# Performance work log

Measured on AMD Instinct MI355X. Metric: run time of the kernel, lower is better.

Reference implementation:

```python
import jax, jax.numpy as jnp
import numpy as np

L, D, H, DH, W, G, FF = 2, 768, 12, 64, 256, 64, 3072  # W = one-sided window (attention_window=512)
B, S = 2, 4096
NEG = -1e9


def setup_inputs() -> dict:
    key = jax.random.key(0)
    ks = jax.random.split(key, 16)
    inp = {}
    inp['hidden_states'] = jax.random.normal(ks[0], (B, S, D), jnp.float32)
    # HF Longformer convention: <0 masked, >0 global, 0 local. First G tokens are global.
    inp['attention_mask'] = jnp.zeros((B, S), jnp.float32).at[:, :G].set(1.0)
    inp['padding_len'] = 0
    inp['level_hierarchy'] = 0
    def w(k, shape):
        return (jax.random.normal(k, shape, jnp.float32) * 0.02)
    for i, n in enumerate(['Wq', 'Wk', 'Wv', 'Wqg', 'Wkg', 'Wvg', 'Wo']):
        inp[n] = w(ks[1 + i], (L, D, D))
        inp['b' + n[1:].lower()] = jnp.zeros((L, D), jnp.float32)
    inp['Wi'] = w(ks[8], (L, D, FF)); inp['bi'] = jnp.zeros((L, FF), jnp.float32)
    inp['Wo2'] = w(ks[9], (L, FF, D)); inp['bo2'] = jnp.zeros((L, D), jnp.float32)
    for n in ['ln1', 'ln2']:
        inp[n + '_g'] = jnp.ones((L, D), jnp.float32)
        inp[n + '_b'] = jnp.zeros((L, D), jnp.float32)
    return inp


def _ln(x, g, b):
    mu = jnp.mean(x, -1, keepdims=True)
    var = jnp.mean(jnp.square(x - mu), -1, keepdims=True)
    return (x - mu) * jax.lax.rsqrt(var + 1e-5) * g + b


def _chunk3(x, nc, w):
    # x: [..., S, d] -> [..., nc, 3w, d]: keys of chunks (c-1, c, c+1), zero-padded at the ends
    shp = x.shape
    xr = x.reshape(shp[:-2] + (nc, w, shp[-1]))
    pad = [(0, 0)] * xr.ndim
    pad[-3] = (1, 1)
    xp = jnp.pad(xr, pad)
    return jnp.concatenate([xp[..., :-2, :, :], xp[..., 1:-1, :, :], xp[..., 2:, :, :]], axis=-2)


def _layer(h, mask, Wq, bq, Wk, bk, Wv, bv, Wqg, bqg, Wkg, bkg, Wvg, bvg,
           Wo, bo, ln1_g, ln1_b, Wi, bi, Wo2, bo2, ln2_g, ln2_b):
    Bb, Ss, Dd = h.shape
    nc = Ss // W
    scale = 1.0 / np.sqrt(DH)
    def heads(x):
        return x.reshape(Bb, Ss, H, DH).transpose(0, 2, 1, 3)  # [B,H,S,dh]
    q = heads(h @ Wq + bq) * scale
    k = heads(h @ Wk + bk)
    v = heads(h @ Wv + bv)
    # --- sliding-window (banded) attention, chunked ---
    qc = q.reshape(Bb, H, nc, W, DH)
    k3 = _chunk3(k, nc, W)  # [B,H,nc,3W,dh]
    v3 = _chunk3(v, nc, W)
    local = jnp.einsum('bhcid,bhcjd->bhcij', qc, k3)  # [B,H,nc,W,3W]
    i = jnp.arange(W)[:, None]
    j = jnp.arange(3 * W)[None, :]
    band_ok = jnp.abs(j - W - i) <= W                              # [W,3W]
    keypos = jnp.arange(nc)[:, None, None] * W + (j - W)[None]     # [nc,1,3W]
    in_range = (keypos >= 0) & (keypos < Ss)
    # masked and global keys are removed from the windowed attention (handled via global cols)
    key_local = _chunk3((mask == 0).astype(h.dtype)[..., None], nc, W)[..., 0] > 0.5  # [B,nc,3W]
    valid = band_ok[None, None] & in_range[None] & key_local[:, :, None, :]  # [B,nc,W,3W]
    local = jnp.where(valid[:, None], local, NEG)
    # --- global key columns (every token attends to the G global tokens) ---
    kg, vg = k[:, :, :G], v[:, :, :G]
    sg = jnp.einsum('bhsd,bhgd->bhsg', q, kg).reshape(Bb, H, nc, W, G)
    probs = jax.nn.softmax(jnp.concatenate([sg, local], axis=-1), axis=-1)
    pg, pl = probs[..., :G], probs[..., G:]
    out = (jnp.einsum('bhcig,bhgd->bhcid', pg, vg)
           + jnp.einsum('bhcij,bhcjd->bhcid', pl, v3)).reshape(Bb, H, Ss, DH)
    # --- global token rows: full attention with dedicated global projections ---
    qg = heads(h @ Wqg + bqg)[:, :, :G] * scale
    kgf = heads(h @ Wkg + bkg)
    vgf = heads(h @ Wvg + bvg)
    add = jnp.where(mask < 0, NEG, 0.0)[:, None, None, :]
    pgl = jax.nn.softmax(jnp.einsum('bhgd,bhsd->bhgs', qg, kgf) + add, axis=-1)
    out = out.at[:, :, :G].set(jnp.einsum('bhgs,bhsd->bhgd', pgl, vgf))
    out = jnp.where((mask < 0)[:, None, :, None], 0.0, out)
    attn = out.transpose(0, 2, 1, 3).reshape(Bb, Ss, Dd) @ Wo + bo
    h = _ln(attn + h, ln1_g, ln1_b)
    ff = jax.nn.gelu(h @ Wi + bi, approximate=False) @ Wo2 + bo2
    return _ln(ff + h, ln2_g, ln2_b)


def reference(hidden_states, attention_mask, padding_len, level_hierarchy,
              Wq, bq, Wk, bk, Wv, bv, Wqg, bqg, Wkg, bkg, Wvg, bvg,
              Wo, bo, ln1_g, ln1_b, Wi, bi, Wo2, bo2, ln2_g, ln2_b):
    h = hidden_states
    for l in range(L):
        h = _layer(h, attention_mask,
                   Wq[l], bq[l], Wk[l], bk[l], Wv[l], bv[l],
                   Wqg[l], bqg[l], Wkg[l], bkg[l], Wvg[l], bvg[l],
                   Wo[l], bo[l], ln1_g[l], ln1_b[l],
                   Wi[l], bi[l], Wo2[l], bo2[l], ln2_g[l], ln2_b[l])
    if padding_len > 0:
        h = h[:, :-padding_len]
    return h
```

## Files before the change

### kernel.cpp

```cpp
#include <hip/hip_runtime.h>

#define B_ 2
#define S_ 4096
#define D_ 768
#define H_ 12
#define DH_ 64
#define W_ 256
#define G_ 64
#define FF_ 3072
#define L_ 2
#define M_ (B_*S_)
#define NEGV -1e9f
#define NSPLIT 16

typedef short bf16x8 __attribute__((ext_vector_type(8)));
typedef float f32x4 __attribute__((ext_vector_type(4)));
typedef unsigned short u16;
typedef unsigned short u16x4 __attribute__((ext_vector_type(4)));

__device__ __forceinline__ u16 f2bf(float f) {
  union { float f; unsigned u; } a; a.f = f;
  unsigned r = a.u + 0x7FFFu + ((a.u >> 16) & 1u);
  return (u16)(r >> 16);
}
__device__ __forceinline__ float b2f(u16 u) {
  union { unsigned u; float f; } a; a.u = ((unsigned)u) << 16;
  return a.f;
}

__device__ __forceinline__ f32x4 mfma16(bf16x8 a, bf16x8 b, f32x4 c) {
  return __builtin_amdgcn_mfma_f32_16x16x32_bf16(a, b, c, 0, 0, 0);
}

__device__ __forceinline__ void gload16(const u16* g, u16* l) {
  __builtin_amdgcn_global_load_lds((const __attribute__((address_space(1))) void*)g,
                                   (__attribute__((address_space(3))) void*)l, 16, 0, 0);
}

__device__ __forceinline__ int xcd_swz(int bid, int nwg) {
  if ((nwg & 7) == 0) {
    int cpx = nwg >> 3;
    bid = (bid & 7) * cpx + (bid >> 3);
  }
  return bid;
}

struct Ptr7 { const float* p[7]; };
__global__ __launch_bounds__(256) void wtrans7(Ptr7 in, u16* __restrict__ out) {
  __shared__ float tile[32][33];
  int z = blockIdx.z;
  int slab = z >> 1, l = z & 1;
  const float* src = in.p[slab] + (size_t)l * D_ * D_;
  u16* dst = out + (size_t)z * D_ * D_;
  int k0 = blockIdx.y * 32, n0 = blockIdx.x * 32;
  int tx = threadIdx.x, ty = threadIdx.y;
#pragma unroll
  for (int i = 0; i < 4; i++)
    tile[ty + i*8][tx] = src[(size_t)(k0 + ty + i*8) * D_ + n0 + tx];
  __syncthreads();
#pragma unroll
  for (int i = 0; i < 4; i++)
    dst[(size_t)(n0 + ty + i*8) * D_ + k0 + tx] = f2bf(tile[tx][ty + i*8]);
}

__global__ __launch_bounds__(256) void wtrans(const float* __restrict__ in,
                                              u16* __restrict__ out, int K, int N) {
  __shared__ float tile[32][33];
  size_t base = (size_t)blockIdx.z * K * N;
  int k0 = blockIdx.y * 32, n0 = blockIdx.x * 32;
  int tx = threadIdx.x, ty = threadIdx.y;
#pragma unroll
  for (int i = 0; i < 4; i++)
    tile[ty + i*8][tx] = in[base + (size_t)(k0 + ty + i*8) * N + n0 + tx];
  __syncthreads();
#pragma unroll
  for (int i = 0; i < 4; i++)
    out[base + (size_t)(n0 + ty + i*8) * K + k0 + tx] = f2bf(tile[tx][ty + i*8]);
}

__global__ __launch_bounds__(256) void conv_b(const float* __restrict__ in,
                                              u16* __restrict__ outb, int n4) {
  int i = blockIdx.x * 256 + threadIdx.x;
  if (i >= n4) return;
  float4 v = ((const float4*)in)[i];
  u16x4 o;
  o[0] = f2bf(v.x); o[1] = f2bf(v.y); o[2] = f2bf(v.z); o[3] = f2bf(v.w);
  ((u16x4*)outb)[i] = o;
}

template <int MODE>
__device__ __forceinline__ float epi_post(float v) {
  if (MODE == 2) return v * 0.125f;
  if (MODE == 3) {
    float y = 0.79788456f * (v + 0.044715f * v * v * v);
    float e = __expf(fminf(2.f * y, 20.f));
    return v * e / (e + 1.f);
  }
  return v;
}

struct Bias5 { const float* p[5]; };

template <int MODE, int NW>
__global__ __launch_bounds__(512, 1) void gemm256(const u16* __restrict__ A,
                                                  const u16* __restrict__ Wbase,
                                                  Bias5 bp,
                                                  u16* __restrict__ OutBase,
                                                  int Kdim, int Nstride, int l) {
  __shared__ u16 sA[2][256 * 64];
  __shared__ u16 sB[2][256 * 64];
  int gx = gridDim.x;
  int bid = blockIdx.x + blockIdx.y * gx;
  bid = xcd_swz(bid, gx * gridDim.y);
  int bxx = bid % gx, by = bid / gx;
  int bm = by * 256;
  int widx, bn;
  const u16* Bt; u16* Cb; const float* bias;
  if (NW == 5) {
    widx = bxx / 3;
    bn = (bxx % 3) * 256;
    int slab = widx + (widx >= 3 ? 1 : 0);
    Bt = Wbase + ((size_t)slab * L_ + l) * (size_t)D_ * D_;
    Cb = OutBase + (size_t)slab * M_ * D_;
    bias = bp.p[widx];
  } else {
    widx = 0;
    bn = bxx * 256;
    Bt = Wbase; Cb = OutBase; bias = bp.p[0];
  }
  int tid = threadIdx.x;
  int lane = tid & 63, wid = tid >> 6;
  int wr = wid >> 2, wc = wid & 3;
  int lr = lane & 15, lg = lane >> 4;

  const u16* srcA[4]; const u16* srcB[4];
#pragma unroll
  for (int i = 0; i < 4; i++) {
    int f = tid + i * 512;
    int row = f >> 3, slot = f & 7;
    int c8 = slot ^ (row & 7);
    srcA[i] = A + (size_t)(bm + row) * Kdim + c8 * 8;
    srcB[i] = Bt + (size_t)(bn + row) * Kdim + c8 * 8;
  }

  f32x4 acc[8][4] = {};
  int nt = Kdim >> 6;

#pragma unroll
  for (int i = 0; i < 4; i++) {
    gload16(srcA[i], &sA[0][(tid + i * 512) * 8]);
    gload16(srcB[i], &sB[0][(tid + i * 512) * 8]);
  }

  for (int kt = 0; kt < nt; kt++) {
    int cur = kt & 1;
    if (kt + 1 < nt) {
      int k1 = (kt + 1) << 6;
#pragma unroll
      for (int i = 0; i < 4; i++) {
        gload16(srcA[i] + k1, &sA[cur ^ 1][(tid + i * 512) * 8]);
        gload16(srcB[i] + k1, &sB[cur ^ 1][(tid + i * 512) * 8]);
      }
      asm volatile("s_waitcnt vmcnt(8)" ::: "memory");
    } else {
      asm volatile("s_waitcnt vmcnt(0)" ::: "memory");
    }
    __builtin_amdgcn_s_barrier();
    __builtin_amdgcn_sched_barrier(0);

#pragma unroll
    for (int qm = 0; qm < 2; qm++) {
      bf16x8 af[4][2];
#pragma unroll
      for (int mi = 0; mi < 4; mi++)
#pragma unroll
        for (int ks = 0; ks < 2; ks++) {
          int row = wr * 128 + qm * 64 + mi * 16 + lr;
          int c8 = ks * 4 + lg;
          af[mi][ks] = *(const bf16x8*)&sA[cur][row * 64 + ((c8 ^ (row & 7)) * 8)];
        }
#pragma unroll
      for (int qn = 0; qn < 2; qn++) {
        bf16x8 bfr[2][2];
#pragma unroll
        for (int nj = 0; nj < 2; nj++)
#pragma unroll
          for (int ks = 0; ks < 2; ks++) {
            int row = wc * 64 + qn * 32 + nj * 16 + lr;
            int c8 = ks * 4 + lg;
            bfr[nj][ks] = *(const bf16x8*)&sB[cur][row * 64 + ((c8 ^ (row & 7)) * 8)];
          }
        __builtin_amdgcn_s_setprio(1);
#pragma unroll
        for (int mi = 0; mi < 4; mi++)
#pragma unroll
          for (int nj = 0; nj < 2; nj++)
#pragma unroll
            for (int ks = 0; ks < 2; ks++)
              acc[qm * 4 + mi][qn * 2 + nj] =
                  mfma16(af[mi][ks], bfr[nj][ks], acc[qm * 4 + mi][qn * 2 + nj]);
        __builtin_amdgcn_s_setprio(0);
      }
    }
    __builtin_amdgcn_sched_barrier(0);
    __builtin_amdgcn_s_barrier();
  }

  int r0 = bm + wr * 128, c0 = bn + wc * 64;
  int cr = (lane >> 4) * 4, cc = lane & 15;
  float sc = (NW == 5 && widx == 0) ? 0.125f : 1.0f;
#pragma unroll
  for (int nj = 0; nj < 4; nj++) {
    int col = c0 + nj * 16 + cc;
    float bv = bias[col];
#pragma unroll
    for (int mi = 0; mi < 8; mi++)
#pragma unroll
      for (int r = 0; r < 4; r++) {
        size_t off = (size_t)(r0 + mi * 16 + cr + r) * Nstride + col;
        Cb[off] = f2bf(epi_post<MODE>((acc[mi][nj][r] + bv) * sc));
      }
  }
}

template <int MODE>
__global__ __launch_bounds__(256) void gemm_pipe(const u16* __restrict__ A,
                                                 const u16* __restrict__ Bt,
                                                 const float* __restrict__ bias,
                                                 u16* __restrict__ Cb,
                                                 int Ndim, int Kdim, int rowTileStride) {
  __shared__ u16 sA[2][4096];
  __shared__ u16 sB[2][4096];
  int gx = gridDim.x;
  int bid = blockIdx.x + blockIdx.y * gx;
  bid = xcd_swz(bid, gx * gridDim.y);
  int bm = (bid / gx) * rowTileStride * 128;
  int bn = (bid % gx) * 128;
  int tid = threadIdx.x;
  int lane = tid & 63, w = tid >> 6;
  int r0w = (w >> 1) * 64, c0w = (w & 1) * 64;
  int lr = lane & 15, lg = lane >> 4;

  int f0 = tid, l0 = f0 >> 3, s0 = (f0 & 7) ^ (l0 & 7);
  int row0 = (l0 << 1) | (s0 >> 2), c0s = (s0 & 3) * 8;
  int f1 = tid + 256, l1 = f1 >> 3, s1 = (f1 & 7) ^ (l1 & 7);
  int row1 = (l1 << 1) | (s1 >> 2), c1s = (s1 & 3) * 8;
  const u16* A0 = A + (size_t)(bm + row0) * Kdim + c0s;
  const u16* A1 = A + (size_t)(bm + row1) * Kdim + c1s;
  const u16* B0 = Bt + (size_t)(bn + row0) * Kdim + c0s;
  const u16* B1 = Bt + (size_t)(bn + row1) * Kdim + c1s;

  int offa[4], offb[4];
#pragma unroll
  for (int i = 0; i < 4; i++) {
    int ra = r0w + i * 16 + lr;
    int la = ra >> 1, sa = ((ra & 1) << 2) | lg;
    offa[i] = la * 64 + (sa ^ (la & 7)) * 8;
    int rb = c0w + i * 16 + lr;
    int lb = rb >> 1, sb = ((rb & 1) << 2) | lg;
    offb[i] = lb * 64 + (sb ^ (lb & 7)) * 8;
  }

  int nt = Kdim >> 5;
  f32x4 acc[4][4] = {};

  gload16(A0, &sA[0][tid * 8]);
  gload16(A1, &sA[0][tid * 8 + 2048]);
  gload16(B0, &sB[0][tid * 8]);
  gload16(B1, &sB[0][tid * 8 + 2048]);

  for (int t = 0; t < nt; t++) {
    int cur = t & 1;
    if (t + 1 < nt) {
      int k1 = (t + 1) << 5;
      gload16(A0 + k1, &sA[cur ^ 1][tid * 8]);
      gload16(A1 + k1, &sA[cur ^ 1][tid * 8 + 2048]);
      gload16(B0 + k1, &sB[cur ^ 1][tid * 8]);
      gload16(B1 + k1, &sB[cur ^ 1][tid * 8 + 2048]);
      asm volatile("s_waitcnt vmcnt(4)" ::: "memory");
    } else {
      asm volatile("s_waitcnt vmcnt(0)" ::: "memory");
    }
    __builtin_amdgcn_s_barrier();
    __builtin_amdgcn_sched_barrier(0);
    bf16x8 a[4], b[4];
#pragma unroll
    for (int i = 0; i < 4; i++) a[i] = *(const bf16x8*)&sA[cur][offa[i]];
#pragma unroll
    for (int j = 0; j < 4; j++) b[j] = *(const bf16x8*)&sB[cur][offb[j]];
#pragma unroll
    for (int i = 0; i < 4; i++)
#pragma unroll
      for (int j = 0; j < 4; j++)
        acc[i][j] = mfma16(a[i], b[j], acc[i][j]);
    __builtin_amdgcn_sched_barrier(0);
    __builtin_amdgcn_s_barrier();
    __builtin_amdgcn_sched_barrier(0);
  }

  int r0 = bm + r0w, c0 = bn + c0w;
  int cr = (lane >> 4) * 4, cc = lane & 15;
#pragma unroll
  for (int j = 0; j < 4; j++) {
    int col = c0 + j * 16 + cc;
    float bv = bias[col];
#pragma unroll
    for (int i = 0; i < 4; i++)
#pragma unroll
      for (int r = 0; r < 4; r++) {
        size_t off = (size_t)(r0 + i * 16 + cr + r) * Ndim + col;
        Cb[off] = f2bf(epi_post<MODE>(acc[i][j][r] + bv));
      }
  }
}

__global__ __launch_bounds__(128) void attn_local(const u16* __restrict__ qb,
                                                  const u16* __restrict__ kb_,
                                                  const u16* __restrict__ vb,
                                                  const float* __restrict__ mask,
                                                  u16* __restrict__ ao) {
  int bid = blockIdx.x + blockIdx.y * gridDim.x;
  bid = xcd_swz(bid, 1536);
  int cx = bid & 63, bh = bid >> 6;
  int c = cx >> 2, sub = cx & 3;
  int b = bh / H_, h = bh % H_;
  int tid = threadIdx.x;
  int w = tid >> 6, lane = tid & 63;
  int lr = lane & 15, lg = lane >> 4;

  __shared__ u16 vtT[64][72];
  __shared__ u16 plds[2][32][72];
  __shared__ unsigned char vflag[576];

  int base_off = sub * 64;
  int kwin0 = c * W_ - W_;
  for (int i = tid; i < 576; i += 128) {
    int kp = kwin0 + base_off + i;
    vflag[i] = (kp >= 0 && kp < S_ && mask[b * S_ + kp] == 0.0f) ? 1 : 0;
  }

  size_t hoff = (size_t)b * S_ * D_ + h * DH_;
  int qrow0 = c * W_ + base_off + w * 32;
  bf16x8 aq[2][2];
#pragma unroll
  for (int fi = 0; fi < 2; fi++)
#pragma unroll
    for (int ks = 0; ks < 2; ks++)
      aq[fi][ks] = *(const bf16x8*)(qb + hoff + (size_t)(qrow0 + fi * 16 + lr) * D_ + ks * 32 + lg * 8);

  float ls[2][4];
  f32x4 o[2][4] = {};
#pragma unroll
  for (int fi = 0; fi < 2; fi++)
#pragma unroll
    for (int r = 0; r < 4; r++) ls[fi][r] = 0.f;

  int stg_k4 = tid >> 3, stg_j = tid & 7;
  int stg_dh0 = stg_j * 8;

  for (int kb = 0; kb <= 9; kb++) {
    int kstart = 0;
    if (kb > 0) {
      kstart = kwin0 + base_off + (kb - 1) * 64;
      if (kstart + 64 <= 0 || kstart >= S_) continue;
    }
    __syncthreads();
    {
#pragma unroll
      for (int p = 0; p < 4; p++) {
        int key = p * 16 + stg_k4;
        int kp = (kb ? kstart : 0) + key;
        bf16x8 row = *(const bf16x8*)(vb + hoff + (size_t)kp * D_ + stg_dh0);
        u16* basep = &vtT[stg_dh0][key ^ (stg_j << 3)];
#pragma unroll
        for (int e = 0; e < 8; e++) basep[e * 72] = (u16)row[e];
      }
    }
    __syncthreads();

    bf16x8 bk0[4], bk1[4];
#pragma unroll
    for (int nj = 0; nj < 4; nj++) {
      int kp = (kb ? kstart : 0) + nj * 16 + lr;
      const u16* ks8 = kb_ + hoff + (size_t)kp * D_ + lg * 8;
      bk0[nj] = *(const bf16x8*)(ks8);
      bk1[nj] = *(const bf16x8*)(ks8 + 32);
    }
    f32x4 sc[2][4];
#pragma unroll
    for (int fi = 0; fi < 2; fi++)
#pragma unroll
      for (int nj = 0; nj < 4; nj++) {
        f32x4 t = {};
        t = mfma16(aq[fi][0], bk0[nj], t);
        t = mfma16(aq[fi][1], bk1[nj], t);
        sc[fi][nj] = t;
      }

    if (kb >= 2 && kb <= 8) {
#pragma unroll
      for (int nj = 0; nj < 4; nj++) {
        bool kv = vflag[(kb - 1) * 64 + nj * 16 + lr] != 0;
#pragma unroll
        for (int fi = 0; fi < 2; fi++)
#pragma unroll
          for (int r = 0; r < 4; r++)
            sc[fi][nj][r] = kv ? sc[fi][nj][r] : NEGV;
      }
    } else if (kb > 0) {
#pragma unroll
      for (int nj = 0; nj < 4; nj++) {
        int fidx = (kb - 1) * 64 + nj * 16 + lr;
        int koff = base_off + fidx;
        bool kv = vflag[fidx] != 0;
#pragma unroll
        for (int fi = 0; fi < 2; fi++)
#pragma unroll
          for (int r = 0; r < 4; r++) {
            int wq = base_off + w * 32 + fi * 16 + lg * 4 + r;
            if (!(kv && koff >= wq && koff <= wq + 2 * W_)) sc[fi][nj][r] = NEGV;
          }
      }
    }

#pragma unroll
    for (int fi = 0; fi < 2; fi++)
#pragma unroll
      for (int r = 0; r < 4; r++) {
        float ps = 0.f;
#pragma unroll
        for (int nj = 0; nj < 4; nj++) {
          float p = __expf(sc[fi][nj][r]);
          sc[fi][nj][r] = p;
          ps += p;
        }
#pragma unroll
        for (int d = 1; d < 16; d <<= 1) ps += __shfl_xor(ps, d);
        ls[fi][r] += ps;
      }

#pragma unroll
    for (int fi = 0; fi < 2; fi++)
#pragma unroll
      for (int nj = 0; nj < 4; nj++)
#pragma unroll
        for (int r = 0; r < 4; r++)
          plds[w][fi * 16 + lg * 4 + r][nj * 16 + lr] = f2bf(sc[fi][nj][r]);
    asm volatile("s_waitcnt lgkmcnt(0)" ::: "memory");
    __builtin_amdgcn_sched_barrier(0);

    bf16x8 ap[2][2];
#pragma unroll
    for (int fi = 0; fi < 2; fi++)
#pragma unroll
      for (int ks = 0; ks < 2; ks++)
        ap[fi][ks] = *(const bf16x8*)&plds[w][fi * 16 + lr][ks * 32 + lg * 8];
#pragma unroll
    for (int dj = 0; dj < 4; dj++) {
      int xr = ((dj * 16 + lr) >> 3) & 7;
#pragma unroll
      for (int ks = 0; ks < 2; ks++) {
        bf16x8 bv = *(const bf16x8*)&vtT[dj * 16 + lr][(ks * 32 + lg * 8) ^ (xr << 3)];
        o[0][dj] = mfma16(ap[0][ks], bv, o[0][dj]);
        o[1][dj] = mfma16(ap[1][ks], bv, o[1][dj]);
      }
    }
  }

#pragma unroll
  for (int fi = 0; fi < 2; fi++)
#pragma unroll
    for (int dj = 0; dj < 4; dj++)
#pragma unroll
      for (int r = 0; r < 4; r++) {
        int row = qrow0 + fi * 16 + lg * 4 + r;
        float v = o[fi][dj][r] / ls[fi][r];
        ao[hoff + (size_t)row * D_ + dj * 16 + lr] = f2bf(v);
      }
}

__global__ __launch_bounds__(128) void attn_gsplit(const u16* __restrict__ qg,
                                                   const u16* __restrict__ kg,
                                                   const u16* __restrict__ vg,
                                                   float* __restrict__ opart,
                                                   float* __restrict__ lpart) {
  int sp = blockIdx.x, bh = blockIdx.y;
  int b = bh / H_, h = bh % H_;
  int tid = threadIdx.x, w = tid >> 6, lane = tid & 63;
  int lr = lane & 15, lg = lane >> 4;
  __shared__ u16 vtT[64][72];
  __shared__ u16 plds[2][32][72];
  size_t hoff = (size_t)b * S_ * D_ + h * DH_;
  int qrow0 = w * 32;
  bf16x8 aq[2][2];
#pragma unroll
  for (int fi = 0; fi < 2; fi++)
#pragma unroll
    for (int ks = 0; ks < 2; ks++)
      aq[fi][ks] = *(const bf16x8*)(qg + hoff + (size_t)(qrow0 + fi * 16 + lr) * D_ + ks * 32 + lg * 8);
  float ls[2][4];
  f32x4 o[2][4] = {};
#pragma unroll
  for (int fi = 0; fi < 2; fi++)
#pragma unroll
    for (int r = 0; r < 4; r++) ls[fi][r] = 0.f;

  int stg_k4 = tid >> 3, stg_j = tid & 7;
  int stg_dh0 = stg_j * 8;

  for (int kb = 0; kb < 4; kb++) {
    int kstart = sp * 256 + kb * 64;
    __syncthreads();
#pragma unroll
    for (int p = 0; p < 4; p++) {
      int key = p * 16 + stg_k4;
      bf16x8 row = *(const bf16x8*)(vg + hoff + (size_t)(kstart + key) * D_ + stg_dh0);
      u16* basep = &vtT[stg_dh0][key ^ (stg_j << 3)];
#pragma unroll
      for (int e = 0; e < 8; e++) basep[e * 72] = (u16)row[e];
    }
    __syncthreads();

    bf16x8 bk0[4], bk1[4];
#pragma unroll
    for (int nj = 0; nj < 4; nj++) {
      const u16* ks8 = kg + hoff + (size_t)(kstart + nj * 16 + lr) * D_ + lg * 8;
      bk0[nj] = *(const bf16x8*)(ks8);
      bk1[nj] = *(const bf16x8*)(ks8 + 32);
    }
    f32x4 sc[2][4];
#pragma unroll
    for (int fi = 0; fi < 2; fi++)
#pragma unroll
      for (int nj = 0; nj < 4; nj++) {
        f32x4 t = {};
        t = mfma16(aq[fi][0], bk0[nj], t);
        t = mfma16(aq[fi][1], bk1[nj], t);
        sc[fi][nj] = t;
      }
#pragma unroll
    for (int fi = 0; fi < 2; fi++)
#pragma unroll
      for (int r = 0; r < 4; r++) {
        float ps = 0.f;
#pragma unroll
        for (int nj = 0; nj < 4; nj++) {
          float p = __expf(sc[fi][nj][r]);
          sc[fi][nj][r] = p;
          ps += p;
        }
#pragma unroll
        for (int d = 1; d < 16; d <<= 1) ps += __shfl_xor(ps, d);
        ls[fi][r] += ps;
      }
#pragma unroll
    for (int fi = 0; fi < 2; fi++)
#pragma unroll
      for (int nj = 0; nj < 4; nj++)
#pragma unroll
        for (int r = 0; r < 4; r++)
          plds[w][fi * 16 + lg * 4 + r][nj * 16 + lr] = f2bf(sc[fi][nj][r]);
    asm volatile("s_waitcnt lgkmcnt(0)" ::: "memory");
    __builtin_amdgcn_sched_barrier(0);
    bf16x8 ap[2][2];
#pragma unroll
    for (int fi = 0; fi < 2; fi++)
#pragma unroll
      for (int ks = 0; ks < 2; ks++)
        ap[fi][ks] = *(const bf16x8*)&plds[w][fi * 16 + lr][ks * 32 + lg * 8];
#pragma unroll
    for (int dj = 0; dj < 4; dj++) {
      int xr = ((dj * 16 + lr) >> 3) & 7;
#pragma unroll
      for (int ks = 0; ks < 2; ks++) {
        bf16x8 bv = *(const bf16x8*)&vtT[dj * 16 + lr][(ks * 32 + lg * 8) ^ (xr << 3)];
        o[0][dj] = mfma16(ap[0][ks], bv, o[0][dj]);
        o[1][dj] = mfma16(ap[1][ks], bv, o[1][dj]);
      }
    }
  }

  size_t pbase = (size_t)(bh * NSPLIT + sp) * 64;
#pragma unroll
  for (int fi = 0; fi < 2; fi++)
#pragma unroll
    for (int r = 0; r < 4; r++) {
      int row = qrow0 + fi * 16 + lg * 4 + r;
      if (lr == 0) lpart[pbase + row] = ls[fi][r];
#pragma unroll
      for (int dj = 0; dj < 4; dj++)
        opart[(pbase + row) * 64 + dj * 16 + lr] = o[fi][dj][r];
    }
}

__global__ __launch_bounds__(256) void attn_gcombine(const float* __restrict__ opart,
                                                     const float* __restrict__ lpart,
                                                     u16* __restrict__ ao) {
  int bh = blockIdx.x;
  int b = bh / H_, h = bh % H_;
  int t = threadIdx.x;
  __shared__ float lt[64];
  if (t < 64) {
    float lsum = 0.f;
#pragma unroll
    for (int sp = 0; sp < NSPLIT; sp++)
      lsum += lpart[(size_t)(bh * NSPLIT + sp) * 64 + t];
    lt[t] = lsum;
  }
  __syncthreads();
  int row = t >> 2, c0 = (t & 3) * 16;
  float acc[16] = {};
  for (int sp = 0; sp < NSPLIT; sp++) {
    const float* op = opart + ((size_t)(bh * NSPLIT + sp) * 64 + row) * 64 + c0;
#pragma unroll
    for (int j = 0; j < 16; j++) acc[j] += op[j];
  }
  float inv = 1.f / lt[row];
  size_t hoff = (size_t)b * S_ * D_ + h * DH_;
#pragma unroll
  for (int j = 0; j < 16; j++)
    ao[hoff + (size_t)row * D_ + c0 + j] = f2bf(acc[j] * inv);
}

__global__ __launch_bounds__(192) void ln_b(const u16* __restrict__ x,
                                            const u16* __restrict__ res,
                                            const float* __restrict__ gg,
                                            const float* __restrict__ bb,
                                            u16* __restrict__ outb,
                                            float* __restrict__ outf) {
  int row = blockIdx.x, t = threadIdx.x;
  const u16* xr = x + (size_t)row * D_;
  const u16* rr = res + (size_t)row * D_;
  u16x4 xv = *(const u16x4*)&xr[t * 4];
  u16x4 rv = *(const u16x4*)&rr[t * 4];
  float v[4];
#pragma unroll
  for (int e = 0; e < 4; e++) v[e] = b2f(xv[e]) + b2f(rv[e]);
  __shared__ float sha[3], shb[3];
  float s = v[0] + v[1] + v[2] + v[3];
#pragma unroll
  for (int d = 1; d < 64; d <<= 1) s += __shfl_xor(s, d);
  if ((t & 63) == 0) sha[t >> 6] = s;
  __syncthreads();
  float mu = (sha[0] + sha[1] + sha[2]) * (1.f / 768.f);
  float dd[4], s2 = 0.f;
#pragma unroll
  for (int e = 0; e < 4; e++) { dd[e] = v[e] - mu; s2 += dd[e] * dd[e]; }
#pragma unroll
  for (int d = 1; d < 64; d <<= 1) s2 += __shfl_xor(s2, d);
  if ((t & 63) == 0) shb[t >> 6] = s2;
  __syncthreads();
  float var = (shb[0] + shb[1] + shb[2]) * (1.f / 768.f);
  float rs = rsqrtf(var + 1e-5f);
  float4 gv = *(const float4*)&gg[t * 4];
  float4 bv = *(const float4*)&bb[t * 4];
  float y0 = dd[0] * rs * gv.x + bv.x;
  float y1 = dd[1] * rs * gv.y + bv.y;
  float y2 = dd[2] * rs * gv.z + bv.z;
  float y3 = dd[3] * rs * gv.w + bv.w;
  u16x4 ov;
  ov[0] = f2bf(y0); ov[1] = f2bf(y1); ov[2] = f2bf(y2); ov[3] = f2bf(y3);
  *(u16x4*)&outb[(size_t)row * D_ + t * 4] = ov;
  if (outf) {
    float4 of = {y0, y1, y2, y3};
    *(float4*)&outf[(size_t)row * D_ + t * 4] = of;
  }
}

extern "C" void kernel_launch(void* const* d_in, const int* in_sizes, int n_in,
                              void* d_out, int out_size, void* d_ws, size_t ws_size,
                              hipStream_t stream) {
  (void)in_sizes; (void)n_in; (void)out_size; (void)ws_size;
  const float* hidden = (const float*)d_in[0];
  const float* mask   = (const float*)d_in[1];
  const float* Wq  = (const float*)d_in[4];   const float* bq  = (const float*)d_in[5];
  const float* Wk  = (const float*)d_in[6];   const float* bk  = (const float*)d_in[7];
  const float* Wv  = (const float*)d_in[8];   const float* bv  = (const float*)d_in[9];
  const float* Wqg = (const float*)d_in[10];  const float* bqg = (const float*)d_in[11];
  const float* Wkg = (const float*)d_in[12];  const float* bkg = (const float*)d_in[13];
  const float* Wvg = (const float*)d_in[14];  const float* bvg = (const float*)d_in[15];
  const float* Wo  = (const float*)d_in[16];  const float* bo  = (const float*)d_in[17];
  const float* Wi  = (const float*)d_in[18];  const float* bi  = (const float*)d_in[19];
  const float* Wo2 = (const float*)d_in[20];  const float* bo2 = (const float*)d_in[21];
  const float* ln1g = (const float*)d_in[22]; const float* ln1b = (const float*)d_in[23];
  const float* ln2g = (const float*)d_in[24]; const float* ln2b = (const float*)d_in[25];

  char* ws = (char*)d_ws;
  size_t off = 0;
  auto alloc = [&](size_t bytes) -> void* {
    void* p = ws + off;
    off += (bytes + 255) & ~(size_t)255;
    return p;
  };
  const size_t DD = (size_t)D_ * D_;
  const size_t DF = (size_t)D_ * FF_;
  u16* Wt = (u16*)alloc((7 * L_ * DD + 2 * L_ * DF) * 2);
  u16* wqg_t = Wt + 3 * L_ * DD;
  u16* wo_t  = Wt + 6 * L_ * DD;
  u16* wi_t  = Wt + 7 * L_ * DD;
  u16* wo2_t = Wt + 7 * L_ * DD + L_ * DF;

  u16* X0 = (u16*)alloc((size_t)M_ * D_ * 2);
  u16* X1 = (u16*)alloc((size_t)M_ * D_ * 2);
  u16* tb = (u16*)alloc((size_t)M_ * D_ * 2);
  u16* B_bf = (u16*)alloc((size_t)M_ * FF_ * 2);
  u16* qbf  = (u16*)alloc((size_t)M_ * D_ * 2);
  u16* kbf  = (u16*)alloc((size_t)M_ * D_ * 2);
  u16* vbf  = (u16*)alloc((size_t)M_ * D_ * 2);
  u16* qgbf = (u16*)alloc((size_t)M_ * D_ * 2);
  u16* kgbf = (u16*)alloc((size_t)M_ * D_ * 2);
  u16* vgbf = (u16*)alloc((size_t)M_ * D_ * 2);
  u16* aobf = (u16*)alloc((size_t)M_ * D_ * 2);
  float* opart = (float*)alloc((size_t)B_ * H_ * NSPLIT * 64 * 64 * 4);
  float* lpart = (float*)alloc((size_t)B_ * H_ * NSPLIT * 64 * 4);

  dim3 tb32(32, 8);
  Ptr7 wp;
  wp.p[0] = Wq; wp.p[1] = Wk; wp.p[2] = Wv; wp.p[3] = Wqg;
  wp.p[4] = Wkg; wp.p[5] = Wvg; wp.p[6] = Wo;
  wtrans7<<<dim3(24, 24, 14), tb32, 0, stream>>>(wp, Wt);
  wtrans<<<dim3(96, 24, 2), tb32, 0, stream>>>(Wi,  wi_t,  D_, FF_);
  wtrans<<<dim3(24, 96, 2), tb32, 0, stream>>>(Wo2, wo2_t, FF_, D_);

  conv_b<<<(M_ * D_ / 4 + 255) / 256, 256, 0, stream>>>(hidden, X0, M_ * D_ / 4);

  for (int l = 0; l < L_; l++) {
    size_t wdd = (size_t)l * DD;
    size_t wdf = (size_t)l * DF;
    dim3 g64(6, 64), g2(6, 2);

    Bias5 bp;
    bp.p[0] = bq  + l * D_;
    bp.p[1] = bk  + l * D_;
    bp.p[2] = bv  + l * D_;
    bp.p[3] = bkg + l * D_;
    bp.p[4] = bvg + l * D_;
    gemm256<1, 5><<<dim3(15, 32), 512, 0, stream>>>(X0, Wt, bp, qbf, D_, D_, l);
    gemm_pipe<2><<<g2, 256, 0, stream>>>(X0, wqg_t + wdd, bqg + l * D_, qgbf, D_, D_, 32);

    attn_local<<<dim3((S_ / W_) * 4, B_ * H_), 128, 0, stream>>>(qbf, kbf, vbf, mask, aobf);
    attn_gsplit<<<dim3(NSPLIT, B_ * H_), 128, 0, stream>>>(qgbf, kgbf, vgbf, opart, lpart);
    attn_gcombine<<<B_ * H_, 256, 0, stream>>>(opart, lpart, aobf);

    gemm_pipe<1><<<g64, 256, 0, stream>>>(aobf, wo_t + wdd, bo + l * D_, tb, D_, D_, 1);
    ln_b<<<M_, 192, 0, stream>>>(tb, X0, ln1g + l * D_, ln1b + l * D_, X1, nullptr);

    Bias5 bpi; bpi.p[0] = bi + l * FF_;
    gemm256<3, 1><<<dim3(12, 32), 512, 0, stream>>>(X1, wi_t + wdf, bpi, B_bf, D_, FF_, 0);
    gemm_pipe<1><<<g64, 256, 0, stream>>>(B_bf, wo2_t + wdf, bo2 + l * D_, tb, D_, FF_, 1);

    ln_b<<<M_, 192, 0, stream>>>(tb, X1, ln2g + l * D_, ln2b + l * D_, X0,
                                 (l == L_ - 1) ? (float*)d_out : nullptr);
  }
}
```

Baseline: 751.1 us.

## Restructure gemm256 into eight-phase ping-pong pipeline with interleaved half-tile loads

Replaces the simple double-buffered K loop of the 256x256 GEMM with a kernel that unrolls two K tiles into eight MFMA phases. Each phase issues half-tile global-to-LDS loads for upcoming tiles between fragment reads and MFMA bursts, so memory traffic is spread across the compute instead of issued in one burst. Barriers and waitcnts are placed per phase. Launch bounds change to 2 blocks per CU, which caps register use and may cause spills or contention. The per-phase barriers add sync overhead, and the waitcnt ordering is delicate, so a mistake could produce races.

Result: faster. 731.2 us (-2.6%).

```diff
diff --git a/kernel.cpp b/kernel.cpp
--- a/kernel.cpp
+++ b/kernel.cpp
@@ -101,14 +101,31 @@
 
 struct Bias5 { const float* p[5]; };
 
+#define VMC4() asm volatile("s_waitcnt vmcnt(4)" ::: "memory")
+#define VMC0() asm volatile("s_waitcnt vmcnt(0)" ::: "memory")
+#define GPH_PRE() do { __builtin_amdgcn_s_barrier(); \
+  asm volatile("s_waitcnt lgkmcnt(0)" ::: "memory"); \
+  __builtin_amdgcn_sched_barrier(0); } while (0)
+#define GPH_PRE_NOLDS() do { __builtin_amdgcn_s_barrier(); \
+  __builtin_amdgcn_sched_barrier(0); } while (0)
+#define GPH_POST() do { __builtin_amdgcn_sched_barrier(0); \
+  __builtin_amdgcn_s_barrier(); } while (0)
+#define GPH_MFMA(AF, BF, QM, QN) do { \
+  __builtin_amdgcn_s_setprio(1); \
+  _Pragma("unroll") for (int mi = 0; mi < 4; mi++) \
+  _Pragma("unroll") for (int nj = 0; nj < 2; nj++) \
+  _Pragma("unroll") for (int ks = 0; ks < 2; ks++) \
+    acc[(QM)*4+mi][(QN)*2+nj] = mfma16(AF[mi][ks], BF[nj][ks], acc[(QM)*4+mi][(QN)*2+nj]); \
+  __builtin_amdgcn_s_setprio(0); } while (0)
+
 template <int MODE, int NW>
-__global__ __launch_bounds__(512, 1) void gemm256(const u16* __restrict__ A,
-                                                  const u16* __restrict__ Wbase,
-                                                  Bias5 bp,
-                                                  u16* __restrict__ OutBase,
-                                                  int Kdim, int Nstride, int l) {
-  __shared__ u16 sA[2][256 * 64];
-  __shared__ u16 sB[2][256 * 64];
+__global__ __launch_bounds__(512, 2) void gemm256p(const u16* __restrict__ A,
+                                                   const u16* __restrict__ Wbase,
+                                                   Bias5 bp,
+                                                   u16* __restrict__ OutBase,
+                                                   int Kdim, int Nstride, int l) {
+  __shared__ u16 sA[2][16384];
+  __shared__ u16 sB[2][16384];
   int gx = gridDim.x;
   int bid = blockIdx.x + blockIdx.y * gx;
   bid = xcd_swz(bid, gx * gridDim.y);
@@ -133,77 +150,74 @@
   int wr = wid >> 2, wc = wid & 3;
   int lr = lane & 15, lg = lane >> 4;
 
-  const u16* srcA[4]; const u16* srcB[4];
-#pragma unroll
-  for (int i = 0; i < 4; i++) {
-    int f = tid + i * 512;
-    int row = f >> 3, slot = f & 7;
-    int c8 = slot ^ (row & 7);
-    srcA[i] = A + (size_t)(bm + row) * Kdim + c8 * 8;
-    srcB[i] = Bt + (size_t)(bn + row) * Kdim + c8 * 8;
-  }
+  int rr0 = tid >> 3, slot0 = tid & 7;
+  int c80 = slot0 ^ (rr0 & 7);
+  const u16* pA = A + (size_t)(bm + rr0) * Kdim + c80 * 8;
+  const u16* pB = Bt + (size_t)(bn + rr0) * Kdim + c80 * 8;
+
+  auto stA = [&](int buf, int h, int kt) {
+    gload16(pA + (size_t)(h * 128) * Kdim + kt * 64, &sA[buf][(h * 1024 + tid) * 8]);
+    gload16(pA + (size_t)(h * 128 + 64) * Kdim + kt * 64, &sA[buf][(h * 1024 + 512 + tid) * 8]);
+  };
+  auto stB = [&](int buf, int h, int kt) {
+    gload16(pB + (size_t)(h * 128) * Kdim + kt * 64, &sB[buf][(h * 1024 + tid) * 8]);
+    gload16(pB + (size_t)(h * 128 + 64) * Kdim + kt * 64, &sB[buf][(h * 1024 + 512 + tid) * 8]);
+  };
+  auto ldA = [&](bf16x8 (&af)[4][2], int c, int qm) {
+#pragma unroll
+    for (int mi = 0; mi < 4; mi++)
+#pragma unroll
+      for (int ks = 0; ks < 2; ks++) {
+        int row = wr * 128 + qm * 64 + mi * 16 + lr;
+        int c8 = ks * 4 + lg;
+        af[mi][ks] = *(const bf16x8*)&sA[c][(row * 8 + (c8 ^ (row & 7))) * 8];
+      }
+  };
+  auto ldB = [&](bf16x8 (&bf)[2][2], int c, int qn) {
+#pragma unroll
+    for (int nj = 0; nj < 2; nj++)
+#pragma unroll
+      for (int ks = 0; ks < 2; ks++) {
+        int row = wc * 64 + qn * 32 + nj * 16 + lr;
+        int c8 = ks * 4 + lg;
+        bf[nj][ks] = *(const bf16x8*)&sB[c][(row * 8 + (c8 ^ (row & 7))) * 8];
+      }
+  };
 
   f32x4 acc[8][4] = {};
   int nt = Kdim >> 6;
 
-#pragma unroll
-  for (int i = 0; i < 4; i++) {
-    gload16(srcA[i], &sA[0][(tid + i * 512) * 8]);
-    gload16(srcB[i], &sB[0][(tid + i * 512) * 8]);
-  }
-
-  for (int kt = 0; kt < nt; kt++) {
-    int cur = kt & 1;
-    if (kt + 1 < nt) {
-      int k1 = (kt + 1) << 6;
-#pragma unroll
-      for (int i = 0; i < 4; i++) {
-        gload16(srcA[i] + k1, &sA[cur ^ 1][(tid + i * 512) * 8]);
-        gload16(srcB[i] + k1, &sB[cur ^ 1][(tid + i * 512) * 8]);
-      }
-      asm volatile("s_waitcnt vmcnt(8)" ::: "memory");
-    } else {
-      asm volatile("s_waitcnt vmcnt(0)" ::: "memory");
-    }
-    __builtin_amdgcn_s_barrier();
-    __builtin_amdgcn_sched_barrier(0);
-
-#pragma unroll
-    for (int qm = 0; qm < 2; qm++) {
-      bf16x8 af[4][2];
-#pragma unroll
-      for (int mi = 0; mi < 4; mi++)
-#pragma unroll
-        for (int ks = 0; ks < 2; ks++) {
-          int row = wr * 128 + qm * 64 + mi * 16 + lr;
-          int c8 = ks * 4 + lg;
-          af[mi][ks] = *(const bf16x8*)&sA[cur][row * 64 + ((c8 ^ (row & 7)) * 8)];
-        }
-#pragma unroll
-      for (int qn = 0; qn < 2; qn++) {
-        bf16x8 bfr[2][2];
-#pragma unroll
-        for (int nj = 0; nj < 2; nj++)
-#pragma unroll
-          for (int ks = 0; ks < 2; ks++) {
-            int row = wc * 64 + qn * 32 + nj * 16 + lr;
-            int c8 = ks * 4 + lg;
-            bfr[nj][ks] = *(const bf16x8*)&sB[cur][row * 64 + ((c8 ^ (row & 7)) * 8)];
-          }
-        __builtin_amdgcn_s_setprio(1);
-#pragma unroll
-        for (int mi = 0; mi < 4; mi++)
-#pragma unroll
-          for (int nj = 0; nj < 2; nj++)
-#pragma unroll
-            for (int ks = 0; ks < 2; ks++)
-              acc[qm * 4 + mi][qn * 2 + nj] =
-                  mfma16(af[mi][ks], bfr[nj][ks], acc[qm * 4 + mi][qn * 2 + nj]);
-        __builtin_amdgcn_s_setprio(0);
-      }
-    }
-    __builtin_amdgcn_sched_barrier(0);
-    __builtin_amdgcn_s_barrier();
+  stA(0, 0, 0); stA(0, 1, 0);
+  stB(0, 0, 0); stB(0, 1, 0);
+  stB(1, 0, 1); stB(1, 1, 1);
+  VMC4();
+  __builtin_amdgcn_s_barrier();
+
+  bf16x8 af[4][2], b0[2][2], b1[2][2];
+  for (int kt = 0; kt < nt; kt += 2) {
+    bool notlast = (kt + 2 < nt);
+    ldA(af, 0, 0); ldB(b0, 0, 0);
+    stA(1, 0, kt + 1);
+    GPH_PRE(); GPH_MFMA(af, b0, 0, 0); GPH_POST();
+    ldB(b1, 0, 1);
+    stA(1, 1, kt + 1);
+    GPH_PRE(); GPH_MFMA(af, b1, 0, 1); GPH_POST();
+    ldA(af, 0, 1);
+    if (notlast) stB(0, 0, kt + 2);
+    GPH_PRE(); GPH_MFMA(af, b0, 1, 0); GPH_POST();
+    if (notlast) { stB(0, 1, kt + 2); VMC4(); } else { VMC0(); }
+    GPH_PRE_NOLDS(); GPH_MFMA(af, b1, 1, 1); GPH_POST();
+    ldA(af, 1, 0); ldB(b0, 1, 0);
+    if (notlast) stA(0, 0, kt + 2);
+    GPH_PRE(); GPH_MFMA(af, b0, 0, 0); GPH_POST();
+    ldB(b1, 1, 1);
+    if (notlast) stA(0, 1, kt + 2);
+    GPH_PRE(); GPH_MFMA(af, b1, 0, 1); GPH_POST();
+    ldA(af, 1, 1);
+    if (notlast) stB(1, 0, kt + 3);
+    GPH_PRE(); GPH_MFMA(af, b0, 1, 0); GPH_POST();
+    if (notlast) { stB(1, 1, kt + 3); VMC4(); } else { VMC0(); }
+    GPH_PRE_NOLDS(); GPH_MFMA(af, b1, 1, 1); GPH_POST();
   }
 
   int r0 = bm + wr * 128, c0 = bn + wc * 64;
@@ -735,7 +749,7 @@
     bp.p[2] = bv  + l * D_;
     bp.p[3] = bkg + l * D_;
     bp.p[4] = bvg + l * D_;
-    gemm256<1, 5><<<dim3(15, 32), 512, 0, stream>>>(X0, Wt, bp, qbf, D_, D_, l);
+    gemm256p<1, 5><<<dim3(15, 32), 512, 0, stream>>>(X0, Wt, bp, qbf, D_, D_, l);
     gemm_pipe<2><<<g2, 256, 0, stream>>>(X0, wqg_t + wdd, bqg + l * D_, qgbf, D_, D_, 32);
 
     attn_local<<<dim3((S_ / W_) * 4, B_ * H_), 128, 0, stream>>>(qbf, kbf, vbf, mask, aobf);
@@ -746,7 +760,7 @@
     ln_b<<<M_, 192, 0, stream>>>(tb, X0, ln1g + l * D_, ln1b + l * D_, X1, nullptr);
 
     Bias5 bpi; bpi.p[0] = bi + l * FF_;
-    gemm256<3, 1><<<dim3(12, 32), 512, 0, stream>>>(X1, wi_t + wdf, bpi, B_bf, D_, FF_, 0);
+    gemm256p<3, 1><<<dim3(12, 32), 512, 0, stream>>>(X1, wi_t + wdf, bpi, B_bf, D_, FF_, 0);
     gemm_pipe<1><<<g64, 256, 0, stream>>>(B_bf, wo2_t + wdf, bo2 + l * D_, tb, D_, FF_, 1);
 
     ln_b<<<M_, 192, 0, stream>>>(tb, X1, ln2g + l * D_, ln2b + l * D_, X0,
```
